# Kernel optimization log

Measured on AMD Instinct MI355X. Metric: run time of the kernel, lower is better.

Reference implementation:

```python
import jax, jax.numpy as jnp
import numpy as np

HEADS = 16
REL_W = 128  # rel_window; rel_proj output size = 2*REL_W + 1 = 257


def setup_inputs() -> dict:
    key = jax.random.key(0)
    k0, k1, k2 = jax.random.split(key, 3)
    b, s, d = 2, 2048, 1024
    hd = d // HEADS
    x = jax.random.normal(k0, (b, s, d), dtype=jnp.float32)
    mask = jnp.ones((b, s), dtype=bool)
    w_qkv = jax.random.normal(k1, (3 * d, d), dtype=jnp.float32) / np.sqrt(d)
    b_qkv = jnp.zeros((3 * d,), dtype=jnp.float32)
    w_rel = jax.random.normal(k2, (2 * REL_W + 1, hd), dtype=jnp.float32) / np.sqrt(hd)
    b_rel = jnp.zeros((2 * REL_W + 1,), dtype=jnp.float32)
    return {"x": x, "mask": mask, "w_qkv": w_qkv, "b_qkv": b_qkv,
            "w_rel": w_rel, "b_rel": b_rel}


def reference(x, mask, w_qkv, b_qkv, w_rel, b_rel):
    b, s, d = x.shape
    hd = d // HEADS
    # to_qkv: [b,s,3d] -> view [b,s,h,3*hd] -> chunk into q,k,v [b,s,h,hd]
    qkv = (x @ w_qkv.T + b_qkv).reshape(b, s, HEADS, 3 * hd)
    q, k, v = jnp.split(qkv, 3, axis=-1)
    q = q.transpose(0, 2, 1, 3)  # [b,h,s,hd]
    k = k.transpose(0, 2, 1, 3)
    v = v.transpose(0, 2, 1, 3)
    scale = jnp.sqrt(jnp.asarray(hd, dtype=x.dtype))  # sqrt(dim/heads)
    content = jnp.einsum('bhik,bhjk->bhij', q, k) / scale  # [b,h,s,s]
    # relative position scores: project queries then gather clamped offsets
    rel = q @ w_rel.T + b_rel  # [b,h,s,2W+1]
    ar = jnp.arange(s)
    offsets = jnp.clip(ar[None, :] - ar[:, None], -REL_W, REL_W) + REL_W  # [s,s]
    pos = jnp.take_along_axis(rel, offsets[None, None, :, :], axis=-1)  # [b,h,s,s]
    scores = content + pos
    scores = jnp.where(mask[:, None, None, :], scores, -jnp.inf)
    attn = jax.nn.softmax(scores, axis=-1)
    out = jnp.einsum('bhij,bhjk->bhik', attn, v)  # [b,h,s,hd]
    return out.transpose(0, 2, 1, 3).reshape(b, s, d)
```

## Files before the change

kernel.cpp:

```cpp
#include <hip/hip_runtime.h>
#include <cstdint>
#include <cstddef>


#define DEV __device__ __forceinline__
using u16    = unsigned short;
using f16x8  = __attribute__((ext_vector_type(8))) _Float16;
using f32x4  = __attribute__((ext_vector_type(4))) float;
using f32x16 = __attribute__((ext_vector_type(16))) float;

DEV f32x4 mfma16(f16x8 a, f16x8 b, f32x4 c) {
  return __builtin_amdgcn_mfma_f32_16x16x32_f16(a, b, c, 0, 0, 0);
}
DEV f32x16 mfma32(f16x8 a, f16x8 b, f32x16 c) {
  return __builtin_amdgcn_mfma_f32_32x32x16_f16(a, b, c, 0, 0, 0);
}
DEV void gload16(const void* g, const void* l) {
  __builtin_amdgcn_global_load_lds((const __attribute__((address_space(1))) void*)g,
                                   (__attribute__((address_space(3))) void*)l,
                                   16, 0, 0);
}
DEV u16 f2h(float f) { _Float16 h = (_Float16)f; return __builtin_bit_cast(u16, h); }
DEV float h2f(u16 u) { return (float)__builtin_bit_cast(_Float16, u); }
DEV uint32_t pkrtz(float a, float b) {
  auto h = __builtin_amdgcn_cvt_pkrtz(a, b);
  return __builtin_bit_cast(uint32_t, h);
}

#if __has_builtin(__builtin_amdgcn_exp2f)
#define EXP2(x) __builtin_amdgcn_exp2f(x)
#else
#define EXP2(x) __expf((x) * 0.6931471805599453f)
#endif
#define LOG2E 1.4426950408889634f

__global__ __launch_bounds__(256) void cvt_all(
    const float* __restrict__ x, const float* __restrict__ wq,
    const float* __restrict__ wr, u16* __restrict__ xb,
    u16* __restrict__ wb, u16* __restrict__ wrelb) {
  int i = (blockIdx.x * 256 + threadIdx.x) * 4;
  if (i < 4194304) {
    float4 v = *(const float4*)(x + i);
    uint32_t a = f2h(v.x) | ((uint32_t)f2h(v.y) << 16);
    uint32_t b = f2h(v.z) | ((uint32_t)f2h(v.w) << 16);
    *(uint2*)(xb + i) = make_uint2(a, b);
  } else if (i < 7340032) {
    int j = i - 4194304;
    float4 v = *(const float4*)(wq + j);
    uint32_t a = f2h(v.x) | ((uint32_t)f2h(v.y) << 16);
    uint32_t b = f2h(v.z) | ((uint32_t)f2h(v.w) << 16);
    *(uint2*)(wb + j) = make_uint2(a, b);
  } else if (i < 7357440) {
    int j = i - 7340032;
#pragma unroll
    for (int e = 0; e < 4; ++e) {
      int r = (j + e) >> 6, c = (j + e) & 63;
      wrelb[j + e] = (r < 257) ? f2h(wr[r * 64 + c]) : (u16)0;
    }
  }
}

__global__ __launch_bounds__(256) void qkv_gemm(
    const u16* __restrict__ xb, const u16* __restrict__ wb,
    const float* __restrict__ bqkv,
    u16* __restrict__ qb, u16* __restrict__ kb, u16* __restrict__ vb) {
  __shared__ __align__(16) u16 lA[128 * 32];
  __shared__ __align__(16) u16 lB[128 * 32];
  const int tid = threadIdx.x, l = tid & 63, w = tid >> 6;
  const int lr = l & 15, lg = l >> 4;
  const int sw = (blockIdx.x & 7) * 96 + (blockIdx.x >> 3);
  const int m0 = (sw / 24) * 128, n0 = (sw % 24) * 128;
  const int wm = w >> 1, wn = w & 1;
  const int srow = l >> 2, scol = (l & 3) * 8;
  f32x4 acc[4][4] = {};
  for (int k0 = 0; k0 < 1024; k0 += 32) {
    __syncthreads();
#pragma unroll
    for (int r = 0; r < 2; ++r) {
      const int row = r * 64 + w * 16 + srow;
      gload16(xb + (size_t)(m0 + row) * 1024 + k0 + scol,
              (const char*)lA + r * 4096 + w * 1024);
      gload16(wb + (size_t)(n0 + row) * 1024 + k0 + scol,
              (const char*)lB + r * 4096 + w * 1024);
    }
    __syncthreads();
    f16x8 af[4], bfr[4];
#pragma unroll
    for (int mf = 0; mf < 4; ++mf)
      af[mf] = *(const f16x8*)((const char*)lA + (wm * 64 + mf * 16 + lr) * 64 + lg * 16);
#pragma unroll
    for (int nf = 0; nf < 4; ++nf)
      bfr[nf] = *(const f16x8*)((const char*)lB + (wn * 64 + nf * 16 + lr) * 64 + lg * 16);
#pragma unroll
    for (int mf = 0; mf < 4; ++mf)
#pragma unroll
      for (int nf = 0; nf < 4; ++nf)
        acc[mf][nf] = mfma16(af[mf], bfr[nf], acc[mf][nf]);
  }
#pragma unroll
  for (int nf = 0; nf < 4; ++nf) {
    const int cg = n0 + wn * 64 + nf * 16 + lr;
    const int h = cg / 192, t = (cg % 192) >> 6, c = cg & 63;
    const float bias = bqkv[cg];
    u16* dst = (t == 0) ? qb : (t == 1) ? kb : vb;
#pragma unroll
    for (int mf = 0; mf < 4; ++mf) {
#pragma unroll
      for (int j = 0; j < 4; ++j) {
        const int rg = m0 + wm * 64 + mf * 16 + lg * 4 + j;
        const int bb = rg >> 11, sr = rg & 2047;
        const int bh = bb * 16 + h;
        dst[((size_t)bh * 2048 + sr) * 64 + c] = f2h(acc[mf][nf][j] + bias);
      }
    }
  }
}

__global__ __launch_bounds__(256) void vtrans(const u16* __restrict__ vb,
                                              u16* __restrict__ vtb) {
  __shared__ u16 t[128][68];
  const int tid = threadIdx.x;
  const int bh = blockIdx.x >> 4, s0 = (blockIdx.x & 15) * 128;
  const u16* src = vb + ((size_t)bh * 2048 + s0) * 64;
#pragma unroll
  for (int it = 0; it < 8; ++it) {
    const int r = it * 16 + (tid >> 4), c = (tid & 15) * 4;
    *(uint2*)&t[r][c] = *(const uint2*)(src + r * 64 + c);
  }
  __syncthreads();
  const int w = tid >> 6, l = tid & 63;
#pragma unroll
  for (int dd = 0; dd < 16; ++dd) {
    const int d = dd * 4 + w;
    u16* dst = vtb + ((size_t)bh * 64 + d) * 2048 + s0;
#pragma unroll
    for (int sh = 0; sh < 2; ++sh)
      dst[sh * 64 + l] = t[sh * 64 + l][d];
  }
}

__global__ __launch_bounds__(256) void rel_proj(
    const u16* __restrict__ qb, const u16* __restrict__ wrelb,
    const float* __restrict__ brel, u16* __restrict__ relb) {
  __shared__ __align__(16) u16 lw[272 * 72];
  const int tid = threadIdx.x, l = tid & 63, w = tid >> 6;
  const int lr = l & 15, lg = l >> 4;
  for (int i = tid; i < 272 * 8; i += 256) {
    const int r = i >> 3, c = i & 7;
    *(f16x8*)(lw + r * 72 + c * 8) = *(const f16x8*)(wrelb + r * 64 + c * 8);
  }
  __syncthreads();
  const int row0 = blockIdx.x * 64 + w * 16;
  f16x8 aq[2];
#pragma unroll
  for (int kk = 0; kk < 2; ++kk)
    aq[kk] = *(const f16x8*)(qb + (size_t)(row0 + lr) * 64 + kk * 32 + lg * 8);
  f32x4 acc[17] = {};
#pragma unroll
  for (int nt = 0; nt < 17; ++nt)
#pragma unroll
    for (int kk = 0; kk < 2; ++kk) {
      f16x8 bfr = *(const f16x8*)(lw + (nt * 16 + lr) * 72 + kk * 32 + lg * 8);
      acc[nt] = mfma16(aq[kk], bfr, acc[nt]);
    }
#pragma unroll
  for (int nt = 0; nt < 17; ++nt) {
    const int cg = nt * 16 + lr;
    if (cg < 257) {
      const float bias = brel[cg];
#pragma unroll
      for (int j = 0; j < 4; ++j) {
        const int rg = row0 + lg * 4 + j;
        relb[(size_t)rg * 257 + cg] = f2h((acc[nt][j] + bias) * LOG2E);
      }
    }
  }
}

__global__ __launch_bounds__(256) void attn_kernel(
    const u16* __restrict__ qb, const u16* __restrict__ kb,
    const u16* __restrict__ vtb, const u16* __restrict__ relb,
    float* __restrict__ out) {
  __shared__ __align__(16) u16 lK[2][64 * 64];
  __shared__ __align__(16) u16 lV[2][64 * 64];
  __shared__ __align__(16) u16 lP[4][32 * 72];
  const int tid = threadIdx.x, l = tid & 63, w = tid >> 6;
  const int q = l & 31, hi = l >> 5;
  const int bid = blockIdx.x;
  const int i8 = bid >> 3;
  const int bh = (bid & 7) * 4 + (i8 & 3);
  const int q0 = (i8 >> 2) * 128 + w * 32;
  const int qrow = q0 + q;
  const float CS = 0.125f * LOG2E;

  f16x8 aq[4];
#pragma unroll
  for (int kkw = 0; kkw < 4; ++kkw)
    aq[kkw] = *(const f16x8*)(qb + ((size_t)bh * 2048 + qrow) * 64 + kkw * 16 + hi * 8);

  const u16* relrow = relb + ((size_t)bh * 2048 + qrow) * 257;
  const float cL = h2f(relrow[0]), cR = h2f(relrow[256]);

  float mi = -1e30f, li = 0.f;
  f32x16 oacc[2] = {};

  u16* lPw = lP[w];
  const int sn = w * 8 + (l >> 3);
  const int sc = (l & 7) ^ (l >> 3);

  auto STAGE = [&](int nb, int kt) {
    const int key0 = kt * 64;
#pragma unroll
    for (int r = 0; r < 2; ++r) {
      const int n = r * 32 + sn;
      gload16(kb + ((size_t)bh * 2048 + key0 + n) * 64 + sc * 8,
              (const char*)lK + nb * 8192 + r * 4096 + w * 1024);
      gload16(vtb + ((size_t)(bh * 64 + n)) * 2048 + key0 + sc * 8,
              (const char*)lV + nb * 8192 + r * 4096 + w * 1024);
    }
  };

  int cur = 0;
  STAGE(0, 0);
  for (int kt = 0; kt < 32; ++kt) {
    __syncthreads();
    if (kt < 31) STAGE(cur ^ 1, kt + 1);

    const char* Kb = (const char*)lK + cur * 8192;
    const char* Vb = (const char*)lV + cur * 8192;
    const int key0 = kt * 64;

    f32x16 sa[2] = {};
    __builtin_amdgcn_s_setprio(1);
#pragma unroll
    for (int s = 0; s < 2; ++s)
#pragma unroll
      for (int kkw = 0; kkw < 4; ++kkw) {
        f16x8 ak = *(const f16x8*)(Kb + (s * 32 + q) * 128 +
                                   (((kkw * 2 + hi) ^ (l & 7)) * 16));
        sa[s] = mfma32(ak, aq[kkw], sa[s]);
      }
    __builtin_amdgcn_s_setprio(0);

    if (key0 <= q0 - 192) {
#pragma unroll
      for (int s = 0; s < 2; ++s)
#pragma unroll
        for (int m = 0; m < 16; ++m) sa[s][m] = sa[s][m] * CS + cL;
    } else if (key0 >= q0 + 160) {
#pragma unroll
      for (int s = 0; s < 2; ++s)
#pragma unroll
        for (int m = 0; m < 16; ++m) sa[s][m] = sa[s][m] * CS + cR;
    } else {
#pragma unroll
      for (int s = 0; s < 2; ++s)
#pragma unroll
        for (int m = 0; m < 16; ++m) {
          const int key = key0 + s * 32 + (m & 3) + 8 * (m >> 2) + 4 * hi;
          int off = key - qrow;
          off = off < -128 ? -128 : (off > 128 ? 128 : off);
          sa[s][m] = sa[s][m] * CS + h2f(relrow[off + 128]);
        }
    }

    float pm = -1e30f;
#pragma unroll
    for (int s = 0; s < 2; ++s)
#pragma unroll
      for (int m = 0; m < 16; ++m) pm = fmaxf(pm, sa[s][m]);
    pm = fmaxf(pm, __shfl_xor(pm, 32));
    if (!__all(pm - mi <= 8.f)) {
      const float mnew = fmaxf(mi, pm);
      const float a = EXP2(mi - mnew);
      li *= a;
#pragma unroll
      for (int ot = 0; ot < 2; ++ot)
#pragma unroll
        for (int m = 0; m < 16; ++m) oacc[ot][m] *= a;
      mi = mnew;
    }
    float ls = 0.f;
#pragma unroll
    for (int s = 0; s < 2; ++s)
#pragma unroll
      for (int m = 0; m < 16; ++m) {
        const float p = EXP2(sa[s][m] - mi);
        sa[s][m] = p;
        ls += p;
      }
    li += ls;

#pragma unroll
    for (int s = 0; s < 2; ++s)
#pragma unroll
      for (int t = 0; t < 4; ++t) {
        uint2 pw;
        pw.x = pkrtz(sa[s][4 * t + 0], sa[s][4 * t + 1]);
        pw.y = pkrtz(sa[s][4 * t + 2], sa[s][4 * t + 3]);
        *(uint2*)(lPw + q * 72 + s * 32 + t * 8 + hi * 4) = pw;
      }
    f16x8 bp[4];
#pragma unroll
    for (int w4 = 0; w4 < 4; ++w4)
      bp[w4] = *(const f16x8*)(lPw + q * 72 + w4 * 16 + hi * 8);

    __builtin_amdgcn_s_setprio(1);
#pragma unroll
    for (int w4 = 0; w4 < 4; ++w4)
#pragma unroll
      for (int ot = 0; ot < 2; ++ot) {
        f16x8 av = *(const f16x8*)(Vb + (ot * 32 + q) * 128 +
                                   (((w4 * 2 + hi) ^ (l & 7)) * 16));
        oacc[ot] = mfma32(av, bp[w4], oacc[ot]);
      }
    __builtin_amdgcn_s_setprio(0);
    cur ^= 1;
  }

  li += __shfl_xor(li, 32);
  const int b = bh >> 4, h = bh & 15;
  const float inv = 1.0f / li;
  const size_t rowb = ((size_t)b * 2048 + qrow) * 1024 + h * 64;
#pragma unroll
  for (int ot = 0; ot < 2; ++ot)
#pragma unroll
    for (int t = 0; t < 4; ++t) {
      float4 o;
      o.x = oacc[ot][4 * t + 0] * inv;
      o.y = oacc[ot][4 * t + 1] * inv;
      o.z = oacc[ot][4 * t + 2] * inv;
      o.w = oacc[ot][4 * t + 3] * inv;
      *(float4*)(out + rowb + ot * 32 + t * 8 + hi * 4) = o;
    }
}

extern "C" void kernel_launch(void* const* d_in, const int* in_sizes, int n_in,
                              void* d_out, int out_size, void* d_ws, size_t ws_size,
                              hipStream_t stream) {
  const float* x     = (const float*)d_in[0];
  const float* w_qkv = (const float*)d_in[2];
  const float* b_qkv = (const float*)d_in[3];
  const float* w_rel = (const float*)d_in[4];
  const float* b_rel = (const float*)d_in[5];
  float* out = (float*)d_out;

  char* ws = (char*)d_ws;
  u16* xb    = (u16*)(ws);
  u16* wb    = (u16*)(ws +  8388608);
  u16* wrelb = (u16*)(ws + 14680064);
  u16* qb    = (u16*)(ws + 14714880);
  u16* kb    = (u16*)(ws + 23103488);
  u16* vtb   = (u16*)(ws + 31492096);
  u16* relb  = (u16*)(ws + 39880704);
  u16* vb    = relb;

  cvt_all<<<7185, 256, 0, stream>>>(x, w_qkv, w_rel, xb, wb, wrelb);
  qkv_gemm<<<768, 256, 0, stream>>>(xb, wb, b_qkv, qb, kb, vb);
  vtrans<<<512, 256, 0, stream>>>(vb, vtb);
  rel_proj<<<1024, 256, 0, stream>>>(qb, wrelb, b_rel, relb);
  attn_kernel<<<512, 256, 0, stream>>>(qb, kb, vtb, relb, out);
}
```

Measured before the change: 254.1 us.

## Triple-buffer K/V tiles, prefetch rel-bias early, and pass P via lane shuffles

The K/V staging moves from double to triple buffering with a prefetch distance of two tiles. A per-iteration __syncthreads is replaced by an explicit s_waitcnt vmcnt plus s_barrier, so loads for the next tile stay in flight during compute. Relative-bias values for the diagonal band are loaded into registers before the QK MFMAs to hide their global-load latency. The P tile no longer round-trips through per-wave LDS; it is rearranged into MFMA B-operand layout with __shfl_xor across the half-waves. This trades more LDS for K/V and more register use for less LDS traffic and fewer stalls, and it relies on the hand-written vmcnt count being correct.

```diff
diff --git a/kernel.cpp b/kernel.cpp
--- a/kernel.cpp
+++ b/kernel.cpp
@@ -181,9 +181,8 @@
     const u16* __restrict__ qb, const u16* __restrict__ kb,
     const u16* __restrict__ vtb, const u16* __restrict__ relb,
     float* __restrict__ out) {
-  __shared__ __align__(16) u16 lK[2][64 * 64];
-  __shared__ __align__(16) u16 lV[2][64 * 64];
-  __shared__ __align__(16) u16 lP[4][32 * 72];
+  __shared__ __align__(16) u16 lK[3][64 * 64];
+  __shared__ __align__(16) u16 lV[3][64 * 64];
   const int tid = threadIdx.x, l = tid & 63, w = tid >> 6;
   const int q = l & 31, hi = l >> 5;
   const int bid = blockIdx.x;
@@ -204,7 +203,6 @@
   float mi = -1e30f, li = 0.f;
   f32x16 oacc[2] = {};
 
-  u16* lPw = lP[w];
   const int sn = w * 8 + (l >> 3);
   const int sc = (l & 7) ^ (l >> 3);
 
@@ -220,15 +218,36 @@
     }
   };
 
-  int cur = 0;
   STAGE(0, 0);
+  STAGE(1, 1);
+
   for (int kt = 0; kt < 32; ++kt) {
-    __syncthreads();
-    if (kt < 31) STAGE(cur ^ 1, kt + 1);
+    const int cur = kt % 3;
+    if (kt < 31) asm volatile("s_waitcnt vmcnt(4)\n\ts_barrier" ::: "memory");
+    else         asm volatile("s_waitcnt vmcnt(0)\n\ts_barrier" ::: "memory");
+
+    const int key0 = kt * 64;
+    const bool bandL = key0 <= q0 - 192, bandR = key0 >= q0 + 160;
+
+    u16 rl[2][16];
+    if (!bandL && !bandR) {
+#pragma unroll
+      for (int s = 0; s < 2; ++s)
+#pragma unroll
+        for (int m = 0; m < 16; ++m) {
+          const int key = key0 + s * 32 + (m & 3) + 8 * (m >> 2) + 4 * hi;
+          int off = key - qrow;
+          off = off < -128 ? -128 : (off > 128 ? 128 : off);
+          rl[s][m] = relrow[off + 128];
+        }
+    }
+#if __has_builtin(__builtin_amdgcn_sched_barrier)
+    __builtin_amdgcn_sched_barrier(0);
+#endif
+    if (kt < 30) STAGE((kt + 2) % 3, kt + 2);
 
     const char* Kb = (const char*)lK + cur * 8192;
     const char* Vb = (const char*)lV + cur * 8192;
-    const int key0 = kt * 64;
 
     f32x16 sa[2] = {};
     __builtin_amdgcn_s_setprio(1);
@@ -242,12 +261,12 @@
       }
     __builtin_amdgcn_s_setprio(0);
 
-    if (key0 <= q0 - 192) {
+    if (bandL) {
 #pragma unroll
       for (int s = 0; s < 2; ++s)
 #pragma unroll
         for (int m = 0; m < 16; ++m) sa[s][m] = sa[s][m] * CS + cL;
-    } else if (key0 >= q0 + 160) {
+    } else if (bandR) {
 #pragma unroll
       for (int s = 0; s < 2; ++s)
 #pragma unroll
@@ -256,12 +275,8 @@
 #pragma unroll
       for (int s = 0; s < 2; ++s)
 #pragma unroll
-        for (int m = 0; m < 16; ++m) {
-          const int key = key0 + s * 32 + (m & 3) + 8 * (m >> 2) + 4 * hi;
-          int off = key - qrow;
-          off = off < -128 ? -128 : (off > 128 ? 128 : off);
-          sa[s][m] = sa[s][m] * CS + h2f(relrow[off + 128]);
-        }
+        for (int m = 0; m < 16; ++m)
+          sa[s][m] = sa[s][m] * CS + h2f(rl[s][m]);
     }
 
     float pm = -1e30f;
@@ -291,31 +306,37 @@
       }
     li += ls;
 
+    uint32_t pka[2][4][2];
 #pragma unroll
     for (int s = 0; s < 2; ++s)
 #pragma unroll
       for (int t = 0; t < 4; ++t) {
-        uint2 pw;
-        pw.x = pkrtz(sa[s][4 * t + 0], sa[s][4 * t + 1]);
-        pw.y = pkrtz(sa[s][4 * t + 2], sa[s][4 * t + 3]);
-        *(uint2*)(lPw + q * 72 + s * 32 + t * 8 + hi * 4) = pw;
-      }
-    f16x8 bp[4];
-#pragma unroll
-    for (int w4 = 0; w4 < 4; ++w4)
-      bp[w4] = *(const f16x8*)(lPw + q * 72 + w4 * 16 + hi * 8);
+        pka[s][t][0] = pkrtz(sa[s][4 * t + 0], sa[s][4 * t + 1]);
+        pka[s][t][1] = pkrtz(sa[s][4 * t + 2], sa[s][4 * t + 3]);
+      }
 
     __builtin_amdgcn_s_setprio(1);
 #pragma unroll
-    for (int w4 = 0; w4 < 4; ++w4)
+    for (int w4 = 0; w4 < 4; ++w4) {
+      const int s = w4 >> 1, tb = (w4 & 1) * 2;
+      const uint32_t own0 = hi ? pka[s][tb + 1][0] : pka[s][tb][0];
+      const uint32_t own1 = hi ? pka[s][tb + 1][1] : pka[s][tb][1];
+      const uint32_t snd0 = hi ? pka[s][tb][0] : pka[s][tb + 1][0];
+      const uint32_t snd1 = hi ? pka[s][tb][1] : pka[s][tb + 1][1];
+      const uint32_t rcv0 = __shfl_xor(snd0, 32);
+      const uint32_t rcv1 = __shfl_xor(snd1, 32);
+      uint4 bw;
+      bw.x = hi ? rcv0 : own0;  bw.y = hi ? rcv1 : own1;
+      bw.z = hi ? own0 : rcv0;  bw.w = hi ? own1 : rcv1;
+      const f16x8 bp = __builtin_bit_cast(f16x8, bw);
 #pragma unroll
       for (int ot = 0; ot < 2; ++ot) {
         f16x8 av = *(const f16x8*)(Vb + (ot * 32 + q) * 128 +
                                    (((w4 * 2 + hi) ^ (l & 7)) * 16));
-        oacc[ot] = mfma32(av, bp[w4], oacc[ot]);
-      }
+        oacc[ot] = mfma32(av, bp, oacc[ot]);
+      }
+    }
     __builtin_amdgcn_s_setprio(0);
-    cur ^= 1;
   }
 
   li += __shfl_xor(li, 32);
```

Measured after the change: 262.1 us. 3.1% more time.
